# Performance work log

Measured on AMD Instinct MI355X. Metric: run time of the kernel, lower is better.

Reference implementation:

```python
import jax, jax.numpy as jnp
import numpy as np
import math

B, H, N, D = 2, 16, 8192, 64
NUM_PROJS = 7
BLOCK = 256   # key block size
SAMPLE = 256  # number of sampled columns


def _gray_perm(n):
    # AngularLSH._unit_hamming_distance_array: Gray-code ordering of 2**n buckets
    a = np.array([0, 1], dtype=np.int32)
    for i in range(1, n):
        a = np.concatenate([a, a[::-1] + 2 ** i])
    return a

PERM = jnp.asarray(_gray_perm(NUM_PROJS))
ENC = jnp.asarray(2 ** np.arange(NUM_PROJS), dtype=jnp.int32)


def lsh_hash(x, proj_dir):
    # sign-bit angular LSH, then Gray-code remap so nearby buckets share bits
    bits = (jnp.einsum('bhnd,dr->bhnr', x, proj_dir) > 0).astype(jnp.int32)
    bin_ids = (bits * ENC).sum(-1)
    return PERM[bin_ids]


def take_seq(x, idx):
    # gather along the sequence axis (axis=2); idx is [B,H,M]
    return jnp.take_along_axis(x, idx[..., None], axis=2)


def setup_inputs() -> dict:
    key = jax.random.key(0)
    ks = jax.random.split(key, 5)
    return {
        'query': jax.random.normal(ks[0], (B, H, N, D), jnp.float32),
        'key': jax.random.normal(ks[1], (B, H, N, D), jnp.float32),
        'value': jax.random.normal(ks[2], (B, H, N, D), jnp.float32),
        'proj_dir': jax.random.normal(ks[3], (D + 1, NUM_PROJS), jnp.float32),
        'sampled_set': jax.random.randint(ks[4], (B, H, SAMPLE), 0, N),
    }


def reference(query, key, value, proj_dir, sampled_set):
    scale = D ** -0.5

    # asymmetric MIPS transform: key gets sqrt(max||k||^2 - ||k||^2), query gets 0
    k_norm = jnp.linalg.norm(key, axis=-1)                 # [B,H,N]
    k_max = jnp.max(k_norm, axis=-1, keepdims=True)        # [B,H,1]
    k_extra = jnp.sqrt(jnp.maximum(k_max ** 2 - k_norm ** 2, 0.0))
    key_aug = jnp.concatenate([key, k_extra[..., None]], axis=-1)
    query_aug = jnp.concatenate([query, jnp.zeros_like(query[..., :1])], axis=-1)

    # stable sort by LSH bucket; inverse permutation to un-sort queries at the end
    q_idx = jnp.argsort(lsh_hash(query_aug, proj_dir), axis=2, stable=True)
    k_idx = jnp.argsort(lsh_hash(key_aug, proj_dir), axis=2, stable=True)
    q_idx_inv = jnp.argsort(q_idx, axis=2, stable=True)

    q_s = take_seq(query, q_idx)
    k_s = take_seq(key, k_idx)
    v_s = take_seq(value, k_idx)

    nb = N // BLOCK      # number of key blocks (N divisible by BLOCK here)
    qbs = N // nb        # query block size

    # 1) block-diagonal exact attention over LSH-sorted blocks
    qb = q_s.reshape(B, H, nb, qbs, D)
    kb = k_s.reshape(B, H, nb, BLOCK, D)
    vb = v_s.reshape(B, H, nb, BLOCK, D)
    s_blk = jnp.einsum('bhgqd,bhgkd->bhgqk', qb, kb) * scale
    lse_blk = jax.nn.logsumexp(s_blk, axis=-1)             # [B,H,nb,qbs]
    attn_blk = jnp.einsum('bhgqk,bhgkd->bhgqd', jax.nn.softmax(s_blk, axis=-1), vb)
    attn_blk = attn_blk.reshape(B, H, N, D)
    lse_blk = lse_blk.reshape(B, H, N, 1)

    # 2) residual via uniformly sampled columns; mask out columns already in the
    #    query's own diagonal block to avoid double counting
    k_sub = take_seq(k_s, sampled_set)                     # [B,H,S,D]
    v_sub = take_seq(v_s, sampled_set)
    q_blk_id = jnp.arange(N) // qbs                        # [N]
    covered = q_blk_id[None, None, :, None] == (sampled_set // BLOCK)[:, :, None, :]
    bias = jnp.where(covered, jnp.finfo(q_s.dtype).min, 0.0)
    s_res = jnp.einsum('bhnd,bhsd->bhns', q_s, k_sub) * scale + bias
    # importance weight n_key/sample_size applied in log-space (approximate_unsampled)
    lse_res = jax.nn.logsumexp(s_res, axis=-1, keepdims=True) + math.log(N / SAMPLE)
    attn_res = jnp.einsum('bhns,bhsd->bhnd', jax.nn.softmax(s_res, axis=-1), v_sub)

    # add_self_attentions: merge the two softmax estimates in log-space
    c = 1.0 / (1.0 + jnp.exp(lse_res - lse_blk))
    attn = c * attn_blk + (1.0 - c) * attn_res

    # un-sort rows back to the original query order
    attn = take_seq(attn, q_idx_inv)
    return attn
```

## Files before the change

kernel.cpp:

```cpp
#include <hip/hip_runtime.h>
#include <hip/hip_bf16.h>
#include <math.h>

#define BD 2
#define HD 16
#define NSEQ 8192
#define DDIM 64
#define NPROJ 7
#define KBLK 256
#define NSAMP 256
#define NBH (BD*HD)
#define NB (NSEQ/KBLK)

typedef short bf16x8 __attribute__((ext_vector_type(8)));
typedef short bf16x4 __attribute__((ext_vector_type(4)));
typedef float f32x4 __attribute__((ext_vector_type(4)));

__device__ __forceinline__ unsigned int pk2bf(float a, float b) {
    union { __hip_bfloat162 h; unsigned int u; } t;
    t.h = __float22bfloat162_rn(make_float2(a, b));
    return t.u;
}

__global__ __launch_bounds__(256) void prelude_kernel(const float* __restrict__ q,
                                                      const float* __restrict__ k,
                                                      const float* __restrict__ pd,
                                                      float* __restrict__ kdots,
                                                      unsigned int* __restrict__ kmax_bits,
                                                      unsigned char* __restrict__ qh) {
    __shared__ float pds[(DDIM+1)*NPROJ];
    __shared__ float red[256];
    const int tid = threadIdx.x;
    for (int i = tid; i < (DDIM+1)*NPROJ; i += 256) pds[i] = pd[i];
    __syncthreads();

    const int lin = blockIdx.x * 256 + tid;
    const int bh = lin >> 13;

    float acc[NPROJ];
    float4 xv[16];

    {
        const float4* xp = (const float4*)(q + (size_t)lin * DDIM);
        #pragma unroll
        for (int j = 0; j < 16; ++j) xv[j] = xp[j];
        #pragma unroll
        for (int r = 0; r < NPROJ; ++r) acc[r] = 0.f;
        #pragma unroll
        for (int j = 0; j < 16; ++j) {
            float xs[4] = {xv[j].x, xv[j].y, xv[j].z, xv[j].w};
            #pragma unroll
            for (int c = 0; c < 4; ++c) {
                const int d = j*4 + c;
                #pragma unroll
                for (int r = 0; r < NPROJ; ++r) acc[r] += xs[c] * pds[d*NPROJ + r];
            }
        }
        int bin = 0;
        #pragma unroll
        for (int r = 0; r < NPROJ; ++r) bin |= (acc[r] > 0.f) << r;
        qh[lin] = (unsigned char)(bin ^ (bin >> 1));
    }

    float nr;
    {
        const float4* xp = (const float4*)(k + (size_t)lin * DDIM);
        #pragma unroll
        for (int j = 0; j < 16; ++j) xv[j] = xp[j];
        #pragma unroll
        for (int r = 0; r < NPROJ; ++r) acc[r] = 0.f;
        #pragma unroll
        for (int j = 0; j < 16; ++j) {
            float xs[4] = {xv[j].x, xv[j].y, xv[j].z, xv[j].w};
            #pragma unroll
            for (int c = 0; c < 4; ++c) {
                const int d = j*4 + c;
                #pragma unroll
                for (int r = 0; r < NPROJ; ++r) acc[r] += xs[c] * pds[d*NPROJ + r];
            }
        }
        float ss = 0.f;
        #pragma unroll
        for (int j = 0; j < 16; ++j) {
            float4 t = xv[j];
            ss += t.x*t.x + t.y*t.y + t.z*t.z + t.w*t.w;
        }
        nr = sqrtf(ss);
        float4* kd = (float4*)(kdots + (size_t)lin * 8);
        kd[0] = make_float4(acc[0], acc[1], acc[2], acc[3]);
        kd[1] = make_float4(acc[4], acc[5], acc[6], nr);
    }

    red[tid] = nr;
    __syncthreads();
    for (int s = 128; s > 0; s >>= 1) {
        if (tid < s) red[tid] = fmaxf(red[tid], red[tid+s]);
        __syncthreads();
    }
    if (tid == 0) atomicMax(&kmax_bits[bh], __float_as_uint(red[0]));
}

__global__ __launch_bounds__(256) void khash_kernel(const float* __restrict__ pd,
                                                    const float* __restrict__ kdots,
                                                    const unsigned int* __restrict__ kmax_bits,
                                                    unsigned char* __restrict__ kh) {
    const int lin = blockIdx.x * 256 + threadIdx.x;
    const int bh = lin >> 13;
    const float4* kd = (const float4*)(kdots + (size_t)lin * 8);
    float4 d0 = kd[0], d1 = kd[1];
    float acc[NPROJ] = {d0.x, d0.y, d0.z, d0.w, d1.x, d1.y, d1.z};
    const float kn = d1.w;
    const float km = __uint_as_float(kmax_bits[bh]);
    const float ex = sqrtf(fmaxf(km*km - kn*kn, 0.f));
    int bin = 0;
    #pragma unroll
    for (int r = 0; r < NPROJ; ++r) {
        acc[r] += ex * pd[DDIM*NPROJ + r];
        bin |= (acc[r] > 0.f) << r;
    }
    kh[lin] = (unsigned char)(bin ^ (bin >> 1));
}

__global__ __launch_bounds__(256) void sort_kernel(const unsigned char* __restrict__ qhash,
                                                   const unsigned char* __restrict__ khash,
                                                   int* __restrict__ qidx,
                                                   int* __restrict__ kidx) {
    __shared__ unsigned char hsh[NSEQ];
    __shared__ unsigned short cnt[128][264];
    __shared__ int base[128];
    __shared__ int wtot[2];
    const int bh = blockIdx.x, tid = threadIdx.x;
    const unsigned char* hash = blockIdx.y ? khash : qhash;
    int* idx = blockIdx.y ? kidx : qidx;

    {
        const uint4* src = (const uint4*)(hash + (size_t)bh * NSEQ);
        uint4* hdst = (uint4*)hsh;
        hdst[tid] = src[tid];
        hdst[tid + 256] = src[tid + 256];
        unsigned int* cz = (unsigned int*)&cnt[0][0];
        for (int i = tid; i < 128*264/2; i += 256) cz[i] = 0;
    }
    __syncthreads();
    {
        const unsigned char* s = hsh + tid*32;
        for (int i = 0; i < 32; ++i) cnt[s[i]][tid]++;
    }
    __syncthreads();

    int sc = 0, vv = 0;
    if (tid < 128) {
        unsigned run = 0;
        uint4* rp = (uint4*)cnt[tid];
        for (int wd = 0; wd < 32; ++wd) {
            uint4 x = rp[wd];
            unsigned v0 = x.x & 0xffffu, v1 = x.x >> 16;
            unsigned v2 = x.y & 0xffffu, v3 = x.y >> 16;
            unsigned v4 = x.z & 0xffffu, v5 = x.z >> 16;
            unsigned v6 = x.w & 0xffffu, v7 = x.w >> 16;
            unsigned p0 = run, p1 = p0+v0, p2 = p1+v1, p3 = p2+v2,
                     p4 = p3+v3, p5 = p4+v4, p6 = p5+v5, p7 = p6+v6;
            run = p7 + v7;
            x.x = p0 | (p1<<16); x.y = p2 | (p3<<16);
            x.z = p4 | (p5<<16); x.w = p6 | (p7<<16);
            rp[wd] = x;
        }
        vv = (int)run;
        sc = vv;
        #pragma unroll
        for (int d = 1; d < 64; d <<= 1) {
            int t = __shfl_up(sc, d, 64);
            if ((tid & 63) >= d) sc += t;
        }
        if ((tid & 63) == 63) wtot[tid >> 6] = sc;
    }
    __syncthreads();
    if (tid < 128) base[tid] = (sc - vv) + (tid >= 64 ? wtot[0] : 0);
    __syncthreads();
    {
        int* dst = idx + (size_t)bh * NSEQ;
        const unsigned char* s = hsh + tid*32;
        for (int i = 0; i < 32; ++i) {
            int h = s[i];
            int c = cnt[h][tid];
            cnt[h][tid] = (unsigned short)(c + 1);
            dst[base[h] + c] = tid*32 + i;
        }
    }
}

#define VSWZ(d) ((((d) >> 1) & 7) << 4)

__global__ __launch_bounds__(256) void respack_kernel(const float* __restrict__ k,
                                                      const float* __restrict__ v,
                                                      const int* __restrict__ samp,
                                                      const int* __restrict__ kidx,
                                                      char* __restrict__ kres,
                                                      char* __restrict__ vres) {
    __shared__ int rows[64];
    const int bh = blockIdx.x, ch = blockIdx.y, tid = threadIdx.x;
    if (tid < 64) rows[tid] = kidx[bh*NSEQ + samp[bh*NSAMP + ch*64 + tid]];
    __syncthreads();
    const size_t basef = (size_t)bh * NSEQ * DDIM;
    char* kimg = kres + (size_t)(bh*4 + ch) * 8192;
    char* vimg = vres + (size_t)(bh*4 + ch) * 8192;

    {
        const int kk = tid & 63, dc = tid >> 6;
        const float* kr = k + basef + (size_t)rows[kk]*DDIM + dc*16;
        float4 f0 = ((const float4*)kr)[0], f1 = ((const float4*)kr)[1];
        float4 f2 = ((const float4*)kr)[2], f3 = ((const float4*)kr)[3];
        union { bf16x8 v8; unsigned int u[4]; } h0, h1;
        h0.u[0] = pk2bf(f0.x,f0.y); h0.u[1] = pk2bf(f0.z,f0.w);
        h0.u[2] = pk2bf(f1.x,f1.y); h0.u[3] = pk2bf(f1.z,f1.w);
        h1.u[0] = pk2bf(f2.x,f2.y); h1.u[1] = pk2bf(f2.z,f2.w);
        h1.u[2] = pk2bf(f3.x,f3.y); h1.u[3] = pk2bf(f3.z,f3.w);
        const int rb = kk*128 + dc*32, sw = (kk & 7) << 4;
        *(bf16x8*)(kimg + ((rb) ^ sw)) = h0.v8;
        *(bf16x8*)(kimg + ((rb + 16) ^ sw)) = h1.v8;
    }
    {
        const int vg = tid & 15, kq = tid >> 4;
        const int r0 = rows[kq*4 + 0], r1 = rows[kq*4 + 1];
        const int r2 = rows[kq*4 + 2], r3 = rows[kq*4 + 3];
        float4 x0 = *(const float4*)(v + basef + (size_t)r0*DDIM + vg*4);
        float4 x1 = *(const float4*)(v + basef + (size_t)r1*DDIM + vg*4);
        float4 x2 = *(const float4*)(v + basef + (size_t)r2*DDIM + vg*4);
        float4 x3 = *(const float4*)(v + basef + (size_t)r3*DDIM + vg*4);
        const float c0[4] = {x0.x, x0.y, x0.z, x0.w};
        const float c1[4] = {x1.x, x1.y, x1.z, x1.w};
        const float c2[4] = {x2.x, x2.y, x2.z, x2.w};
        const float c3[4] = {x3.x, x3.y, x3.z, x3.w};
        #pragma unroll
        for (int j = 0; j < 4; ++j) {
            const int d = vg*4 + j;
            unsigned h01 = pk2bf(c0[j], c1[j]);
            unsigned h23 = pk2bf(c2[j], c3[j]);
            *(uint2*)(vimg + ((d*128 + kq*8) ^ VSWZ(d))) = make_uint2(h01, h23);
        }
    }
}


#define LN32 3.46573590279972f

template<int PHASE>
__device__ __forceinline__ void compute_chunk(
    int ch, int lane,
    const bf16x8 (&qhf)[4][2], const bf16x8 (&qlf)[4][2],
    f32x4 (&O)[4][4], float (&lacc)[4],
    const float* maskF, const char* KhL, const char* VthL) {

    const int lr4 = lane >> 4;
    const int lc  = lane & 15;

    #pragma unroll
    for (int mt = 0; mt < 4; ++mt) {
        const int key = mt*16 + lc;
        const int ksw = (key & 7) << 4;
        bf16x8 ka0 = *(const bf16x8*)(KhL + ((key*128 +  0 + lr4*16) ^ ksw));
        bf16x8 ka1 = *(const bf16x8*)(KhL + ((key*128 + 64 + lr4*16) ^ ksw));
        float4 mk;
        if (PHASE) mk = *(const float4*)(maskF + ch*64 + mt*16 + lr4*4);

        bf16x4 pb[4];
        #pragma unroll
        for (int qt = 0; qt < 4; ++qt) {
            f32x4 c = {0.f, 0.f, 0.f, 0.f};
            c = __builtin_amdgcn_mfma_f32_16x16x32_bf16(ka0, qhf[qt][0], c, 0, 0, 0);
            c = __builtin_amdgcn_mfma_f32_16x16x32_bf16(ka0, qlf[qt][0], c, 0, 0, 0);
            c = __builtin_amdgcn_mfma_f32_16x16x32_bf16(ka1, qhf[qt][1], c, 0, 0, 0);
            c = __builtin_amdgcn_mfma_f32_16x16x32_bf16(ka1, qlf[qt][1], c, 0, 0, 0);
            float e0, e1, e2, e3;
            if (PHASE) {
                e0 = __expf(c[0] + LN32) * mk.x;
                e1 = __expf(c[1] + LN32) * mk.y;
                e2 = __expf(c[2] + LN32) * mk.z;
                e3 = __expf(c[3] + LN32) * mk.w;
            } else {
                e0 = __expf(c[0]); e1 = __expf(c[1]);
                e2 = __expf(c[2]); e3 = __expf(c[3]);
            }
            lacc[qt] += (e0+e1) + (e2+e3);
            union { bf16x4 v4; unsigned int u[2]; } pw;
            pw.u[0] = pk2bf(e0, e1);
            pw.u[1] = pk2bf(e2, e3);
            pb[qt] = pw.v4;
        }

        __builtin_amdgcn_s_setprio(1);
        #pragma unroll
        for (int dt = 0; dt < 4; ++dt) {
            const int d = dt*16 + lc;
            bf16x4 va = *(const bf16x4*)(VthL + ((d*128 + mt*32 + lr4*8) ^ VSWZ(d)));
            #pragma unroll
            for (int qt = 0; qt < 4; ++qt)
                O[qt][dt] = __builtin_amdgcn_mfma_f32_16x16x16bf16_1k(va, pb[qt], O[qt][dt], 0, 0, 0);
        }
        __builtin_amdgcn_s_setprio(0);
    }
}

__global__ __launch_bounds__(256)
__attribute__((amdgpu_waves_per_eu(2, 2)))
void attn_kernel(const float* __restrict__ q,
                 const float* __restrict__ k,
                 const float* __restrict__ v,
                 const int* __restrict__ samp,
                 const int* __restrict__ qidx,
                 const int* __restrict__ kidx,
                 const char* __restrict__ kres,
                 const char* __restrict__ vres,
                 float* __restrict__ out) {
    __shared__ __align__(16) char KB[8192];
    __shared__ __align__(16) char VB[8192];
    __shared__ int qidxL[256];
    __shared__ int kidxL[256];
    __shared__ __align__(16) float maskF[256];

    const int g = blockIdx.x, bh = blockIdx.y;
    const int tid = threadIdx.x;
    const int lane = tid & 63, w = tid >> 6;
    const int lr4 = lane >> 4, lc = lane & 15;
    const size_t basef = (size_t)bh * NSEQ * DDIM;

    qidxL[tid] = qidx[bh*NSEQ + g*KBLK + tid];
    kidxL[tid] = kidx[bh*NSEQ + g*KBLK + tid];
    {
        int sp = samp[bh*NSAMP + tid];
        maskF[tid] = ((sp >> 8) == g) ? 0.f : 1.f;
    }
    __syncthreads();

    bf16x8 qhf[4][2], qlf[4][2];
    #pragma unroll
    for (int qt = 0; qt < 4; ++qt) {
        const int qrow = qidxL[w*64 + qt*16 + lc];
        const float* qp = q + basef + (size_t)qrow*DDIM;
        #pragma unroll
        for (int ks = 0; ks < 2; ++ks) {
            const float* p = qp + ks*32 + lr4*8;
            float4 a = *(const float4*)p;
            float4 b = *(const float4*)(p + 4);
            float xs[8] = {a.x,a.y,a.z,a.w,b.x,b.y,b.z,b.w};
            union { bf16x8 v8; unsigned int u[4]; } hv, lv;
            #pragma unroll
            for (int j = 0; j < 4; ++j) {
                float s0 = xs[2*j]   * 0.125f;
                float s1 = xs[2*j+1] * 0.125f;
                unsigned hp = pk2bf(s0, s1);
                hv.u[j] = hp;
                float l0 = s0 - __uint_as_float(hp << 16);
                float l1 = s1 - __uint_as_float(hp & 0xffff0000u);
                lv.u[j] = pk2bf(l0, l1);
            }
            qhf[qt][ks] = hv.v8; qlf[qt][ks] = lv.v8;
        }
    }

    f32x4 O[4][4];
    #pragma unroll
    for (int a = 0; a < 4; ++a)
        #pragma unroll
        for (int b = 0; b < 4; ++b) O[a][b] = (f32x4){0.f,0.f,0.f,0.f};
    float lacc[4] = {0,0,0,0};

    const int kk = tid & 63, dcw = tid >> 6;
    const int vg = tid & 15, kq = tid >> 4;

    for (int ch = 0; ch < 4; ++ch) {
        __syncthreads();
        {
            const int korig = kidxL[ch*64 + kk];
            const float* kr = k + basef + (size_t)korig*DDIM + dcw*16;
            float4 f0 = ((const float4*)kr)[0], f1 = ((const float4*)kr)[1];
            float4 f2 = ((const float4*)kr)[2], f3 = ((const float4*)kr)[3];
            union { bf16x8 v8; unsigned int u[4]; } h0, h1;
            h0.u[0] = pk2bf(f0.x,f0.y); h0.u[1] = pk2bf(f0.z,f0.w);
            h0.u[2] = pk2bf(f1.x,f1.y); h0.u[3] = pk2bf(f1.z,f1.w);
            h1.u[0] = pk2bf(f2.x,f2.y); h1.u[1] = pk2bf(f2.z,f2.w);
            h1.u[2] = pk2bf(f3.x,f3.y); h1.u[3] = pk2bf(f3.z,f3.w);
            const int rb = kk*128 + dcw*32, sw2 = (kk & 7) << 4;
            *(bf16x8*)(KB + ((rb) ^ sw2)) = h0.v8;
            *(bf16x8*)(KB + ((rb + 16) ^ sw2)) = h1.v8;
        }
        {
            const int r0 = kidxL[ch*64 + kq*4 + 0];
            const int r1 = kidxL[ch*64 + kq*4 + 1];
            const int r2 = kidxL[ch*64 + kq*4 + 2];
            const int r3 = kidxL[ch*64 + kq*4 + 3];
            float4 x0 = *(const float4*)(v + basef + (size_t)r0*DDIM + vg*4);
            float4 x1 = *(const float4*)(v + basef + (size_t)r1*DDIM + vg*4);
            float4 x2 = *(const float4*)(v + basef + (size_t)r2*DDIM + vg*4);
            float4 x3 = *(const float4*)(v + basef + (size_t)r3*DDIM + vg*4);
            const float c0[4] = {x0.x, x0.y, x0.z, x0.w};
            const float c1[4] = {x1.x, x1.y, x1.z, x1.w};
            const float c2[4] = {x2.x, x2.y, x2.z, x2.w};
            const float c3[4] = {x3.x, x3.y, x3.z, x3.w};
            #pragma unroll
            for (int j = 0; j < 4; ++j) {
                const int d = vg*4 + j;
                unsigned h01 = pk2bf(c0[j], c1[j]);
                unsigned h23 = pk2bf(c2[j], c3[j]);
                *(uint2*)(VB + ((d*128 + kq*8) ^ VSWZ(d))) = make_uint2(h01, h23);
            }
        }
        __syncthreads();
        compute_chunk<0>(ch, lane, qhf, qlf, O, lacc, maskF, KB, VB);
    }

    for (int ch = 0; ch < 4; ++ch) {
        __syncthreads();
        {
            const char* ksrc = kres + (size_t)(bh*4 + ch) * 8192 + tid*32;
            const char* vsrc = vres + (size_t)(bh*4 + ch) * 8192 + tid*32;
            float4 a0 = ((const float4*)ksrc)[0];
            float4 a1 = ((const float4*)ksrc)[1];
            float4 b0 = ((const float4*)vsrc)[0];
            float4 b1 = ((const float4*)vsrc)[1];
            *(float4*)(KB + tid*32)      = a0;
            *(float4*)(KB + tid*32 + 16) = a1;
            *(float4*)(VB + tid*32)      = b0;
            *(float4*)(VB + tid*32 + 16) = b1;
        }
        __syncthreads();
        compute_chunk<1>(ch, lane, qhf, qlf, O, lacc, maskF, KB, VB);
    }

    #pragma unroll
    for (int qt = 0; qt < 4; ++qt) {
        lacc[qt] += __shfl_xor(lacc[qt], 16, 64);
        lacc[qt] += __shfl_xor(lacc[qt], 32, 64);
        lacc[qt] = 1.f / lacc[qt];
    }
    float* ob = out + basef;
    #pragma unroll
    for (int qt = 0; qt < 4; ++qt) {
        const int orow = qidxL[w*64 + qt*16 + lc];
        const float f = lacc[qt];
        float* p = ob + (size_t)orow*DDIM + lr4*4;
        #pragma unroll
        for (int dt = 0; dt < 4; ++dt) {
            float4 st = make_float4(O[qt][dt][0]*f, O[qt][dt][1]*f,
                                    O[qt][dt][2]*f, O[qt][dt][3]*f);
            *(float4*)(p + dt*16) = st;
        }
    }
}

extern "C" void kernel_launch(void* const* d_in, const int* in_sizes, int n_in,
                              void* d_out, int out_size, void* d_ws, size_t ws_size,
                              hipStream_t stream) {
    const float* q    = (const float*)d_in[0];
    const float* k    = (const float*)d_in[1];
    const float* v    = (const float*)d_in[2];
    const float* pd   = (const float*)d_in[3];
    const int*   samp = (const int*)d_in[4];
    float* out = (float*)d_out;

    char* ws = (char*)d_ws;
    float*         kdots = (float*)(ws + 0);
    int*           qidx  = (int*)(ws + 0);
    int*           kidx  = (int*)(ws + 1048576);
    char*          kres  = ws + 2097152;
    char*          vres  = ws + 3145728;
    unsigned char* qh    = (unsigned char*)(ws + 8388608);
    unsigned char* kh    = (unsigned char*)(ws + 8650752);
    unsigned int*  kmaxb = (unsigned int*)(ws + 8912896);

    hipMemsetAsync(kmaxb, 0, NBH*sizeof(unsigned int), stream);
    hipLaunchKernelGGL(prelude_kernel, dim3(NBH*NSEQ/256), dim3(256), 0, stream,
                       q, k, pd, kdots, kmaxb, qh);
    hipLaunchKernelGGL(khash_kernel, dim3(NBH*NSEQ/256), dim3(256), 0, stream,
                       pd, kdots, kmaxb, kh);
    hipLaunchKernelGGL(sort_kernel, dim3(NBH, 2), dim3(256), 0, stream, qh, kh, qidx, kidx);
    hipLaunchKernelGGL(respack_kernel, dim3(NBH, 4), dim3(256), 0, stream,
                       k, v, samp, kidx, kres, vres);
    hipLaunchKernelGGL(attn_kernel, dim3(NB, NBH), dim3(256), 0, stream,
                       q, k, v, samp, qidx, kidx, kres, vres, out);
}
```

Before: 156.7 us.

## Double-buffer K/V shared-memory staging across all eight chunks in attention kernel

Merges the block-diagonal and sampled-residual loops into a single unrolled loop of eight chunks. K/V shared buffers become double-buffered so that loading and bf16-converting the next chunk is issued before computing the current one, with one barrier per iteration instead of two. This aims to hide global gather latency behind MFMA work. It doubles LDS use per block, can raise register pressure since loaded values stay live across the compute, and replaces the waves_per_eu attribute with a launch_bounds minimum-blocks hint.

```diff
diff --git a/kernel.cpp b/kernel.cpp
--- a/kernel.cpp
+++ b/kernel.cpp
@@ -301,19 +301,17 @@
     }
 }
 
-__global__ __launch_bounds__(256)
-__attribute__((amdgpu_waves_per_eu(2, 2)))
-void attn_kernel(const float* __restrict__ q,
-                 const float* __restrict__ k,
-                 const float* __restrict__ v,
-                 const int* __restrict__ samp,
-                 const int* __restrict__ qidx,
-                 const int* __restrict__ kidx,
-                 const char* __restrict__ kres,
-                 const char* __restrict__ vres,
-                 float* __restrict__ out) {
-    __shared__ __align__(16) char KB[8192];
-    __shared__ __align__(16) char VB[8192];
+__global__ __launch_bounds__(256, 2) void attn_kernel(const float* __restrict__ q,
+                                                      const float* __restrict__ k,
+                                                      const float* __restrict__ v,
+                                                      const int* __restrict__ samp,
+                                                      const int* __restrict__ qidx,
+                                                      const int* __restrict__ kidx,
+                                                      const char* __restrict__ kres,
+                                                      const char* __restrict__ vres,
+                                                      float* __restrict__ out) {
+    __shared__ __align__(16) char KB[2][8192];
+    __shared__ __align__(16) char VB[2][8192];
     __shared__ int qidxL[256];
     __shared__ int kidxL[256];
     __shared__ __align__(16) float maskF[256];
@@ -331,6 +329,57 @@
         maskF[tid] = ((sp >> 8) == g) ? 0.f : 1.f;
     }
     __syncthreads();
+
+    const int kk = tid & 63, dcw = tid >> 6;
+    const int vg = tid & 15, kq = tid >> 4;
+
+    #define STAGE(CH, B)                                                          \
+    {                                                                             \
+        if ((CH) < 4) {                                                           \
+            const int korig = kidxL[(CH)*64 + kk];                                \
+            const float* kr = k + basef + (size_t)korig*DDIM + dcw*16;            \
+            float4 f0 = ((const float4*)kr)[0], f1 = ((const float4*)kr)[1];      \
+            float4 f2 = ((const float4*)kr)[2], f3 = ((const float4*)kr)[3];      \
+            union { bf16x8 v8; unsigned int u[4]; } h0, h1;                       \
+            h0.u[0] = pk2bf(f0.x,f0.y); h0.u[1] = pk2bf(f0.z,f0.w);               \
+            h0.u[2] = pk2bf(f1.x,f1.y); h0.u[3] = pk2bf(f1.z,f1.w);               \
+            h1.u[0] = pk2bf(f2.x,f2.y); h1.u[1] = pk2bf(f2.z,f2.w);               \
+            h1.u[2] = pk2bf(f3.x,f3.y); h1.u[3] = pk2bf(f3.z,f3.w);               \
+            const int rb = kk*128 + dcw*32, sw2 = (kk & 7) << 4;                  \
+            *(bf16x8*)(KB[B] + ((rb) ^ sw2)) = h0.v8;                             \
+            *(bf16x8*)(KB[B] + ((rb + 16) ^ sw2)) = h1.v8;                        \
+            const int r0 = kidxL[(CH)*64 + kq*4 + 0];                             \
+            const int r1 = kidxL[(CH)*64 + kq*4 + 1];                             \
+            const int r2 = kidxL[(CH)*64 + kq*4 + 2];                             \
+            const int r3 = kidxL[(CH)*64 + kq*4 + 3];                             \
+            float4 x0 = *(const float4*)(v + basef + (size_t)r0*DDIM + vg*4);     \
+            float4 x1 = *(const float4*)(v + basef + (size_t)r1*DDIM + vg*4);     \
+            float4 x2 = *(const float4*)(v + basef + (size_t)r2*DDIM + vg*4);     \
+            float4 x3 = *(const float4*)(v + basef + (size_t)r3*DDIM + vg*4);     \
+            const float c0[4] = {x0.x, x0.y, x0.z, x0.w};                         \
+            const float c1[4] = {x1.x, x1.y, x1.z, x1.w};                         \
+            const float c2[4] = {x2.x, x2.y, x2.z, x2.w};                         \
+            const float c3[4] = {x3.x, x3.y, x3.z, x3.w};                         \
+            _Pragma("unroll")                                                     \
+            for (int j = 0; j < 4; ++j) {                                         \
+                const int d = vg*4 + j;                                           \
+                unsigned h01 = pk2bf(c0[j], c1[j]);                               \
+                unsigned h23 = pk2bf(c2[j], c3[j]);                               \
+                *(uint2*)(VB[B] + ((d*128 + kq*8) ^ VSWZ(d))) = make_uint2(h01, h23); \
+            }                                                                     \
+        } else {                                                                  \
+            const char* ksrc = kres + (size_t)(bh*4 + (CH) - 4) * 8192 + tid*32;  \
+            const char* vsrc = vres + (size_t)(bh*4 + (CH) - 4) * 8192 + tid*32;  \
+            float4 a0 = ((const float4*)ksrc)[0];                                 \
+            float4 a1 = ((const float4*)ksrc)[1];                                 \
+            float4 b0 = ((const float4*)vsrc)[0];                                 \
+            float4 b1 = ((const float4*)vsrc)[1];                                 \
+            *(float4*)(KB[B] + tid*32)      = a0;                                 \
+            *(float4*)(KB[B] + tid*32 + 16) = a1;                                 \
+            *(float4*)(VB[B] + tid*32)      = b0;                                 \
+            *(float4*)(VB[B] + tid*32 + 16) = b1;                                 \
+        }                                                                         \
+    }
 
     bf16x8 qhf[4][2], qlf[4][2];
     #pragma unroll
@@ -365,67 +414,17 @@
         for (int b = 0; b < 4; ++b) O[a][b] = (f32x4){0.f,0.f,0.f,0.f};
     float lacc[4] = {0,0,0,0};
 
-    const int kk = tid & 63, dcw = tid >> 6;
-    const int vg = tid & 15, kq = tid >> 4;
-
-    for (int ch = 0; ch < 4; ++ch) {
+    STAGE(0, 0)
+    __syncthreads();
+
+    #pragma unroll
+    for (int ch = 0; ch < 8; ++ch) {
+        if (ch < 7) STAGE(ch + 1, (ch + 1) & 1)
+        if (ch < 4) compute_chunk<0>(ch,   lane, qhf, qlf, O, lacc, maskF, KB[ch&1], VB[ch&1]);
+        else        compute_chunk<1>(ch-4, lane, qhf, qlf, O, lacc, maskF, KB[ch&1], VB[ch&1]);
         __syncthreads();
-        {
-            const int korig = kidxL[ch*64 + kk];
-            const float* kr = k + basef + (size_t)korig*DDIM + dcw*16;
-            float4 f0 = ((const float4*)kr)[0], f1 = ((const float4*)kr)[1];
-            float4 f2 = ((const float4*)kr)[2], f3 = ((const float4*)kr)[3];
-            union { bf16x8 v8; unsigned int u[4]; } h0, h1;
-            h0.u[0] = pk2bf(f0.x,f0.y); h0.u[1] = pk2bf(f0.z,f0.w);
-            h0.u[2] = pk2bf(f1.x,f1.y); h0.u[3] = pk2bf(f1.z,f1.w);
-            h1.u[0] = pk2bf(f2.x,f2.y); h1.u[1] = pk2bf(f2.z,f2.w);
-            h1.u[2] = pk2bf(f3.x,f3.y); h1.u[3] = pk2bf(f3.z,f3.w);
-            const int rb = kk*128 + dcw*32, sw2 = (kk & 7) << 4;
-            *(bf16x8*)(KB + ((rb) ^ sw2)) = h0.v8;
-            *(bf16x8*)(KB + ((rb + 16) ^ sw2)) = h1.v8;
-        }
-        {
-            const int r0 = kidxL[ch*64 + kq*4 + 0];
-            const int r1 = kidxL[ch*64 + kq*4 + 1];
-            const int r2 = kidxL[ch*64 + kq*4 + 2];
-            const int r3 = kidxL[ch*64 + kq*4 + 3];
-            float4 x0 = *(const float4*)(v + basef + (size_t)r0*DDIM + vg*4);
-            float4 x1 = *(const float4*)(v + basef + (size_t)r1*DDIM + vg*4);
-            float4 x2 = *(const float4*)(v + basef + (size_t)r2*DDIM + vg*4);
-            float4 x3 = *(const float4*)(v + basef + (size_t)r3*DDIM + vg*4);
-            const float c0[4] = {x0.x, x0.y, x0.z, x0.w};
-            const float c1[4] = {x1.x, x1.y, x1.z, x1.w};
-            const float c2[4] = {x2.x, x2.y, x2.z, x2.w};
-            const float c3[4] = {x3.x, x3.y, x3.z, x3.w};
-            #pragma unroll
-            for (int j = 0; j < 4; ++j) {
-                const int d = vg*4 + j;
-                unsigned h01 = pk2bf(c0[j], c1[j]);
-                unsigned h23 = pk2bf(c2[j], c3[j]);
-                *(uint2*)(VB + ((d*128 + kq*8) ^ VSWZ(d))) = make_uint2(h01, h23);
-            }
-        }
-        __syncthreads();
-        compute_chunk<0>(ch, lane, qhf, qlf, O, lacc, maskF, KB, VB);
-    }
-
-    for (int ch = 0; ch < 4; ++ch) {
-        __syncthreads();
-        {
-            const char* ksrc = kres + (size_t)(bh*4 + ch) * 8192 + tid*32;
-            const char* vsrc = vres + (size_t)(bh*4 + ch) * 8192 + tid*32;
-            float4 a0 = ((const float4*)ksrc)[0];
-            float4 a1 = ((const float4*)ksrc)[1];
-            float4 b0 = ((const float4*)vsrc)[0];
-            float4 b1 = ((const float4*)vsrc)[1];
-            *(float4*)(KB + tid*32)      = a0;
-            *(float4*)(KB + tid*32 + 16) = a1;
-            *(float4*)(VB + tid*32)      = b0;
-            *(float4*)(VB + tid*32 + 16) = b1;
-        }
-        __syncthreads();
-        compute_chunk<1>(ch, lane, qhf, qlf, O, lacc, maskF, KB, VB);
-    }
+    }
+    #undef STAGE
 
     #pragma unroll
     for (int qt = 0; qt < 4; ++qt) {
```

Measured after the change: 431.5 us. 175% more time.
